# Performance work log

Measured on AMD Instinct MI355X. Metric: run time of the kernel, lower is better.

## Reference

```python
import jax, jax.numpy as jnp
import numpy as np
import math

B, N, DIM, NH, K, PD = 2, 2048, 512, 8, 32, 16
HD = DIM // NH
LN_EPS = 1e-6  # flax LayerNorm default


def _poincare_dist(x, y, c):
    # x, y broadcast to [B, N, N, PD]; returns [B, N, N]
    diff_norm_sq = jnp.sum((x - y) ** 2, axis=-1)
    x_norm_sq = jnp.sum(x ** 2, axis=-1)
    y_norm_sq = jnp.sum(y ** 2, axis=-1)
    den = (1.0 - c * x_norm_sq) * (1.0 - c * y_norm_sq)
    arg = 1.0 + 2.0 * c * diff_norm_sq / jnp.clip(den, 1e-8)
    safe_arg = jnp.maximum(arg, 1.0 + 1e-7)
    return jnp.arccosh(safe_arg) / jnp.sqrt(c)


def _layernorm(x, scale, bias):
    m = jnp.mean(x, axis=-1, keepdims=True)
    v = jnp.var(x, axis=-1, keepdims=True)
    return (x - m) / jnp.sqrt(v + LN_EPS) * scale + bias


def setup_inputs() -> dict:
    key = jax.random.key(0)
    ks = jax.random.split(key, 12)

    def dense(k, din, dout):
        W = jax.random.normal(k, (din, dout), jnp.float32) / np.sqrt(din).astype(np.float32)
        b = jnp.zeros((dout,), jnp.float32)
        return W, b

    inp = {}
    inp["x"] = jax.random.normal(ks[0], (B, N, DIM), jnp.float32)
    # points inside the unit Poincare ball (c=1)
    inp["positions"] = (jax.random.uniform(ks[1], (B, N, PD), jnp.float32) - 0.5) * 0.2
    inp["c"] = jnp.float32(1.0)
    inp["Wq"], inp["bq"] = dense(ks[2], DIM, DIM)
    inp["Wk"], inp["bk"] = dense(ks[3], DIM, DIM)
    inp["Wv"], inp["bv"] = dense(ks[4], DIM, DIM)
    inp["Wo"], inp["bo"] = dense(ks[5], DIM, DIM)
    inp["W1"], inp["b1"] = dense(ks[6], DIM, 4 * DIM)
    inp["W2"], inp["b2"] = dense(ks[7], 4 * DIM, DIM)
    inp["ln1_scale"] = jnp.ones((DIM,), jnp.float32)
    inp["ln1_bias"] = jnp.zeros((DIM,), jnp.float32)
    inp["ln2_scale"] = jnp.ones((DIM,), jnp.float32)
    inp["ln2_bias"] = jnp.zeros((DIM,), jnp.float32)
    inp["log_tau"] = jnp.zeros((1,), jnp.float32)
    inp["attn_scale"] = jnp.ones((1,), jnp.float32)
    return inp


def reference(x, positions, c, Wq, bq, Wk, bk, Wv, bv, Wo, bo,
              W1, b1, W2, b2, ln1_scale, ln1_bias, ln2_scale, ln2_bias,
              log_tau, attn_scale):
    x_res = x
    x_norm = _layernorm(x, ln1_scale, ln1_bias)

    def heads(W, b):
        return (x_norm @ W + b).reshape(B, N, NH, HD).transpose(0, 2, 1, 3)  # [B,H,N,HD]

    q = heads(Wq, bq)
    k = heads(Wk, bk)
    v = heads(Wv, bv)

    # pairwise hyperbolic distances [B,N,N]
    dist_matrix = _poincare_dist(positions[:, None, :, :], positions[:, :, None, :], c)
    _, top_k_indices = jax.lax.top_k(-dist_matrix, K)  # [B,N,K]

    # gather neighbor K/V: out[b,h,i,j,d] = kv[b,h, idx[b,i,j], d]
    gather = jax.vmap(lambda kv_b, idx_b: kv_b[:, idx_b, :])
    k_gathered = gather(k, top_k_indices)  # [B,H,N,K,HD]
    v_gathered = gather(v, top_k_indices)  # [B,H,N,K,HD]

    feature_scores = jnp.einsum('bhid,bhikd->bhik', q, k_gathered) / math.sqrt(HD)
    gathered_dists = jnp.take_along_axis(dist_matrix, top_k_indices, axis=-1)  # [B,N,K]
    geometric_scores = -gathered_dists[:, None, :, :] / jnp.clip(jnp.exp(log_tau), 1e-8)
    attn_scores = attn_scale * jnp.tanh(feature_scores + geometric_scores)
    attn_weights = jax.nn.softmax(attn_scores, axis=-1)

    attn_output = jnp.einsum('bhik,bhikd->bhid', attn_weights, v_gathered)
    attn_output = attn_output.transpose(0, 2, 1, 3).reshape(B, N, DIM)

    x1 = x_res + attn_output @ Wo + bo
    x2_norm = _layernorm(x1, ln2_scale, ln2_bias)
    ffn = jax.nn.gelu(x2_norm @ W1 + b1) @ W2 + b2  # gelu approximate=True (flax default)
    return x1 + ffn
```

## Files before the change

kernel.cpp:

```cpp
#include <hip/hip_runtime.h>
#include <math.h>

#define B_   2
#define N_   2048
#define DIM_ 512
#define NH_  8
#define HD_  64
#define K_   32
#define PD_  16
#define TOK_ (B_*N_)
#define FFN_ 2048
#define QKV_ (3*DIM_)
#define KV_  1024

typedef __bf16 bf16x8 __attribute__((ext_vector_type(8)));
typedef float  f32x4  __attribute__((ext_vector_type(4)));

__device__ __forceinline__ unsigned short f2bf(float f) {
    unsigned int u = __float_as_uint(f);
    u = (u + 0x7fffu + ((u >> 16) & 1u)) >> 16;
    return (unsigned short)u;
}

__device__ __forceinline__ float bflo(unsigned u) { return __uint_as_float(u << 16); }
__device__ __forceinline__ float bfhi(unsigned u) { return __uint_as_float(u & 0xffff0000u); }

__device__ __forceinline__ float gelu_tanh(float x) {
    float x3 = x * x * x;
    return 0.5f * x * (1.f + tanhf(0.7978845608028654f * (x + 0.044715f * x3)));
}

__device__ __forceinline__ float tanh_fast(float x) {
    float e = __expf(2.f * x);
    return 1.f - 2.f / (e + 1.f);
}

__device__ __forceinline__ int lane_mbcnt(unsigned long long m) {
    return __builtin_amdgcn_mbcnt_hi((unsigned)(m >> 32),
           __builtin_amdgcn_mbcnt_lo((unsigned)m, 0));
}

#define GLOAD_LDS16(g, l) __builtin_amdgcn_global_load_lds(                        \
    (const __attribute__((address_space(1))) unsigned int*)(const void*)(g),       \
    (__attribute__((address_space(3))) unsigned int*)(void*)(l), 16, 0, 0)

template<int EPI, int BM, int BN>
__global__ __launch_bounds__(256)
void gemm_bf16_kernel(const unsigned short* __restrict__ A,
                      const unsigned short* __restrict__ Bt,
                      const float* __restrict__ bias,
                      const float* __restrict__ res,
                      float* __restrict__ Cf,
                      unsigned short* __restrict__ Cb,
                      int N, int Kd)
{
    constexpr int WM = BM / 2;
    constexpr int WN = BN / 2;
    constexpr int FM = WM / 16;
    constexpr int FN = WN / 16;
    constexpr int BUFSZ = (BM + BN) * 64;

    __shared__ __align__(16) unsigned short smem[2 * BUFSZ];

    int t    = threadIdx.x;
    int lane = t & 63;
    int wid  = t >> 6;
    int wm   = wid >> 1, wn = wid & 1;
    int bm0  = blockIdx.y * BM;
    int bn0  = blockIdx.x * BN;
    int quad = lane >> 4;
    int rlo  = lane & 15;

    f32x4 acc[FM][FN] = {};

    auto stage = [&](int buf, int k0) {
        unsigned short* As_ = smem + buf * BUFSZ;
        unsigned short* Bs_ = As_ + BM * 64;
#pragma unroll
        for (int l = 0; l < BM/32; l++) {
            int idx = l*256 + t;
            int r   = idx >> 3;
            int g   = (idx & 7) ^ (r & 7);
            GLOAD_LDS16(A + (size_t)(bm0 + r) * Kd + k0 + g*8, As_ + idx*8);
        }
#pragma unroll
        for (int l = 0; l < BN/32; l++) {
            int idx = l*256 + t;
            int r   = idx >> 3;
            int g   = (idx & 7) ^ (r & 7);
            GLOAD_LDS16(Bt + (size_t)(bn0 + r) * Kd + k0 + g*8, Bs_ + idx*8);
        }
    };

    auto compute = [&](int buf) {
        unsigned short* As_ = smem + buf * BUFSZ;
        unsigned short* Bs_ = As_ + BM * 64;
        bf16x8 af[FM][2], bfr[FN][2];
#pragma unroll
        for (int mi = 0; mi < FM; mi++) {
            int r = wm*WM + mi*16 + rlo;
#pragma unroll
            for (int s = 0; s < 2; s++)
                af[mi][s] = *(const bf16x8*)(As_ + r*64 + ((s*4 + quad) ^ (r & 7))*8);
        }
#pragma unroll
        for (int ni = 0; ni < FN; ni++) {
            int r = wn*WN + ni*16 + rlo;
#pragma unroll
            for (int s = 0; s < 2; s++)
                bfr[ni][s] = *(const bf16x8*)(Bs_ + r*64 + ((s*4 + quad) ^ (r & 7))*8);
        }
#pragma unroll
        for (int s = 0; s < 2; s++)
#pragma unroll
            for (int mi = 0; mi < FM; mi++)
#pragma unroll
                for (int ni = 0; ni < FN; ni++)
                    acc[mi][ni] = __builtin_amdgcn_mfma_f32_16x16x32_bf16(
                        af[mi][s], bfr[ni][s], acc[mi][ni], 0, 0, 0);
    };

    stage(0, 0);
    int buf = 0;
    for (int k0 = 0; k0 < Kd; k0 += 64) {
        __syncthreads();
        if (k0 + 64 < Kd) stage(buf ^ 1, k0 + 64);
        compute(buf);
        buf ^= 1;
    }

#pragma unroll
    for (int mi = 0; mi < FM; mi++) {
#pragma unroll
        for (int ni = 0; ni < FN; ni++) {
            int col = bn0 + wn*WN + ni*16 + rlo;
            float bv = bias[col];
#pragma unroll
            for (int r = 0; r < 4; r++) {
                int row = bm0 + wm*WM + mi*16 + quad*4 + r;
                float val = acc[mi][ni][r] + bv;
                if (EPI == 1) val += res[(size_t)row * N + col];
                if (EPI == 2) {
                    val = gelu_tanh(val);
                    Cb[(size_t)row * N + col] = f2bf(val);
                } else if (EPI == 3) {
                    if (col < DIM_) Cf[(size_t)row * DIM_ + col] = val;
                    else            Cb[(size_t)row * KV_ + (col - DIM_)] = f2bf(val);
                } else {
                    Cf[(size_t)row * N + col] = val;
                }
            }
        }
    }
}

__device__ __forceinline__ void extract_row(const unsigned* rb, unsigned T,
                                            int cnt_lt, int m,
                                            unsigned long long* crow,
                                            int hw, int jbase, int lane)
{
    int ltpos = 0;
#pragma unroll
    for (int tt = 0; tt < 16; tt++) {
        bool is_lt = rb[tt] < T;
        unsigned long long mlt = __ballot(is_lt);
        int p = ltpos + lane_mbcnt(mlt);
        if (is_lt) {
            int j = jbase + (tt >> 2)*256 + lane*4 + (tt & 3);
            crow[hw*K_ + p] = ((unsigned long long)rb[tt] << 32) | (unsigned)j;
        }
        ltpos += __popcll(mlt);
    }
    int eqpos = 0;
#pragma unroll
    for (int jg = 0; jg < 4; jg++) {
        bool iseq[4]; unsigned long long meq[4]; int bel[4];
#pragma unroll
        for (int jj = 0; jj < 4; jj++) {
            iseq[jj] = (rb[jg*4+jj] == T);
            meq[jj]  = __ballot(iseq[jj]);
            bel[jj]  = lane_mbcnt(meq[jj]);
        }
        int lane_prefix = bel[0] + bel[1] + bel[2] + bel[3];
        int within = 0;
#pragma unroll
        for (int jj = 0; jj < 4; jj++) {
            int p = eqpos + lane_prefix + within;
            if (iseq[jj] && p < m) {
                int j = jbase + jg*256 + lane*4 + jj;
                crow[hw*K_ + cnt_lt + p] =
                    ((unsigned long long)rb[jg*4+jj] << 32) | (unsigned)j;
            }
            within += iseq[jj] ? 1 : 0;
        }
        eqpos += __popcll(meq[0]) + __popcll(meq[1]) + __popcll(meq[2]) + __popcll(meq[3]);
    }
}

__global__ __launch_bounds__(256)
void dist_topk_kernel(const float* __restrict__ pos,
                      const float* __restrict__ posT,
                      const float* __restrict__ pos_sq,
                      const float* __restrict__ c_ptr,
                      int* __restrict__ topk_idx, float* __restrict__ topk_dist)
{
    __shared__ unsigned long long cand[4][64];

    int wid  = threadIdx.x >> 6;
    int lane = threadIdx.x & 63;
    int rg   = wid >> 1;
    int hw   = wid & 1;
    int bi0  = blockIdx.x * 4 + rg * 2;
    int b    = bi0 >> 11;
    float c  = *c_ptr;
    float inv_sqrt_c = rsqrtf(c);

    float pi0[16], pi1[16];
    {
        const float4* q0 = (const float4*)(pos + (size_t)bi0 * PD_);
        const float4* q1 = (const float4*)(pos + (size_t)(bi0+1) * PD_);
#pragma unroll
        for (int u = 0; u < 4; u++) {
            float4 a = q0[u];
            pi0[4*u]=a.x; pi0[4*u+1]=a.y; pi0[4*u+2]=a.z; pi0[4*u+3]=a.w;
            float4 e = q1[u];
            pi1[4*u]=e.x; pi1[4*u+1]=e.y; pi1[4*u+2]=e.z; pi1[4*u+3]=e.w;
        }
    }
    float om0 = 1.f - c * pos_sq[bi0];
    float om1 = 1.f - c * pos_sq[bi0+1];

    const float* pT  = posT + (size_t)b * 16 * N_;
    const float* sqb = pos_sq + b * N_;
    int jbase = hw * 1024;
    int j0l   = jbase + lane * 4;

    unsigned rb0[16], rb1[16];
#pragma unroll
    for (int jg = 0; jg < 4; jg++) {
        int j0 = j0l + jg * 256;
        float ax=0,ay=0,az=0,aw=0, bx=0,by=0,bz=0,bw=0;
#pragma unroll
        for (int d = 0; d < 16; d++) {
            float4 v = *(const float4*)(pT + d * N_ + j0);
            float d0x = pi0[d]-v.x, d0y = pi0[d]-v.y, d0z = pi0[d]-v.z, d0w = pi0[d]-v.w;
            ax += d0x*d0x; ay += d0y*d0y; az += d0z*d0z; aw += d0w*d0w;
            float d1x = pi1[d]-v.x, d1y = pi1[d]-v.y, d1z = pi1[d]-v.z, d1w = pi1[d]-v.w;
            bx += d1x*d1x; by += d1y*d1y; bz += d1z*d1z; bw += d1w*d1w;
        }
        float4 sq = *(const float4*)(sqb + j0);
        float da[4]={ax,ay,az,aw}, db[4]={bx,by,bz,bw}, sqa[4]={sq.x,sq.y,sq.z,sq.w};
#pragma unroll
        for (int jj = 0; jj < 4; jj++) {
            float omj  = 1.f - c * sqa[jj];
            float den0 = fmaxf(om0 * omj, 1e-8f);
            float den1 = fmaxf(om1 * omj, 1e-8f);
            rb0[jg*4+jj] = __float_as_uint(fmaxf(1.f + 2.f*c*da[jj]/den0, 1.f+1e-7f));
            rb1[jg*4+jj] = __float_as_uint(fmaxf(1.f + 2.f*c*db[jj]/den1, 1.f+1e-7f));
        }
    }

    unsigned T0, T1;
    {
        unsigned band0 = rb0[0], bor0 = rb0[0], band1 = rb1[0], bor1 = rb1[0];
#pragma unroll
        for (int tt = 1; tt < 16; tt++) {
            band0 &= rb0[tt]; bor0 |= rb0[tt];
            band1 &= rb1[tt]; bor1 |= rb1[tt];
        }
#pragma unroll
        for (int off = 32; off; off >>= 1) {
            band0 &= __shfl_xor(band0, off); bor0 |= __shfl_xor(bor0, off);
            band1 &= __shfl_xor(band1, off); bor1 |= __shfl_xor(bor1, off);
        }
        unsigned df0 = band0 ^ bor0, df1 = band1 ^ bor1;
        int hib0 = df0 ? (31 - __clz(df0)) : -1;
        int hib1 = df1 ? (31 - __clz(df1)) : -1;
        int hib  = hib0 > hib1 ? hib0 : hib1;
        T0 = (hib >= 0) ? (band0 & ~((1u << (hib+1)) - 1u)) : band0;
        T1 = (hib >= 0) ? (band1 & ~((1u << (hib+1)) - 1u)) : band1;
        for (int bit = hib; bit >= 0; --bit) {
            unsigned p0 = T0 | (1u << bit), p1 = T1 | (1u << bit);
            int c0 = 0, c1 = 0;
#pragma unroll
            for (int tt = 0; tt < 16; tt++) {
                c0 += __popcll(__ballot(rb0[tt] < p0));
                c1 += __popcll(__ballot(rb1[tt] < p1));
            }
            if (c0 < K_) T0 = p0;
            if (c1 < K_) T1 = p1;
        }
    }
    int cl0 = 0, cl1 = 0;
#pragma unroll
    for (int tt = 0; tt < 16; tt++) {
        cl0 += __popcll(__ballot(rb0[tt] < T0));
        cl1 += __popcll(__ballot(rb1[tt] < T1));
    }

    extract_row(rb0, T0, cl0, K_ - cl0, cand[rg*2+0], hw, jbase, lane);
    extract_row(rb1, T1, cl1, K_ - cl1, cand[rg*2+1], hw, jbase, lane);
    __syncthreads();

    {
        unsigned long long mykey = cand[wid][lane];
        int rank = 0;
#pragma unroll 8
        for (int M = 0; M < 64; M++)
            rank += (cand[wid][M] < mykey) ? 1 : 0;
        if (rank < K_) {
            int bi = blockIdx.x * 4 + wid;
            topk_idx [(size_t)bi * K_ + rank] = (int)(mykey & 0xffffffffu);
            topk_dist[(size_t)bi * K_ + rank] =
                acoshf(__uint_as_float((unsigned)(mykey >> 32))) * inv_sqrt_c;
        }
    }
}

__global__ void fused_prep_kernel(const float* __restrict__ Wq, const float* __restrict__ Wk,
                            const float* __restrict__ Wv, const float* __restrict__ Wo,
                            const float* __restrict__ W1, const float* __restrict__ W2,
                            const float* __restrict__ bq, const float* __restrict__ bk,
                            const float* __restrict__ bv,
                            unsigned short* __restrict__ qkvWt,
                            unsigned short* __restrict__ WoT,
                            unsigned short* __restrict__ W1T,
                            unsigned short* __restrict__ W2T,
                            float* __restrict__ qkv_b,
                            const float* __restrict__ pos,
                            float* __restrict__ pos_sq,
                            float* __restrict__ posT,
                            const float* __restrict__ x,
                            const float* __restrict__ ln1_scale,
                            const float* __restrict__ ln1_bias,
                            unsigned short* __restrict__ xn)
{
    int id = blockIdx.x;
    int t  = threadIdx.x;

    if (id >= 3094) {
        int wave = (id - 3094) * 4 + (t >> 6);
        int lane = t & 63;
        const float* xr = x + (size_t)wave * DIM_;
        float v[8];
        float s = 0.f;
#pragma unroll
        for (int i = 0; i < 8; i++) { v[i] = xr[lane + i*64]; s += v[i]; }
#pragma unroll
        for (int off = 32; off; off >>= 1) s += __shfl_xor(s, off);
        float mean = s * (1.f / DIM_);
        float vs = 0.f;
#pragma unroll
        for (int i = 0; i < 8; i++) { float d = v[i] - mean; vs += d*d; }
#pragma unroll
        for (int off = 32; off; off >>= 1) vs += __shfl_xor(vs, off);
        float inv = rsqrtf(vs * (1.f / DIM_) + 1e-6f);
        unsigned short* yr = xn + (size_t)wave * DIM_;
#pragma unroll
        for (int i = 0; i < 8; i++) {
            int cc = lane + i*64;
            yr[cc] = f2bf((v[i] - mean) * inv * ln1_scale[cc] + ln1_bias[cc]);
        }
        return;
    }
    if (id >= 3078) {
        int i = (id - 3078) * 256 + t;
        int b = i >> 11, j = i & (N_ - 1);
        const float4* p = (const float4*)(pos + (size_t)i * PD_);
        float4 a0 = p[0], a1 = p[1], a2 = p[2], a3 = p[3];
        float pv[16] = {a0.x,a0.y,a0.z,a0.w, a1.x,a1.y,a1.z,a1.w,
                        a2.x,a2.y,a2.z,a2.w, a3.x,a3.y,a3.z,a3.w};
        float s = 0.f;
#pragma unroll
        for (int d = 0; d < 16; d++) s += pv[d]*pv[d];
        pos_sq[i] = s;
        float* pT = posT + (size_t)b * 16 * N_;
#pragma unroll
        for (int d = 0; d < 16; d++) pT[d * N_ + j] = pv[d];
        return;
    }
    if (id >= 3072) {
        int i = (id - 3072) * 256 + t;
        if (i < DIM_)            qkv_b[i] = bq[i];
        else if (i < 2*DIM_)     qkv_b[i] = bk[i - DIM_];
        else                     qkv_b[i] = bv[i - 2*DIM_];
        return;
    }

    const float* W; unsigned short* Wt; int Kd, Nw, nx, ti;
    if      (id < 256)  { W = Wq; Wt = qkvWt;               Kd = 512;  Nw = 512;  nx = 16; ti = id; }
    else if (id < 512)  { W = Wk; Wt = qkvWt + 512*512;     Kd = 512;  Nw = 512;  nx = 16; ti = id - 256; }
    else if (id < 768)  { W = Wv; Wt = qkvWt + 2*512*512;   Kd = 512;  Nw = 512;  nx = 16; ti = id - 512; }
    else if (id < 1024) { W = Wo; Wt = WoT;                 Kd = 512;  Nw = 512;  nx = 16; ti = id - 768; }
    else if (id < 2048) { W = W1; Wt = W1T;                 Kd = 512;  Nw = 2048; nx = 64; ti = id - 1024; }
    else                { W = W2; Wt = W2T;                 Kd = 2048; Nw = 512;  nx = 16; ti = id - 2048; }

    __shared__ float tile[32][33];
    int n0 = (ti % nx) * 32, k0 = (ti / nx) * 32;
    int tx = t & 31, ty = t >> 5;
#pragma unroll
    for (int i = 0; i < 32; i += 8)
        tile[ty + i][tx] = W[(size_t)(k0 + ty + i) * Nw + n0 + tx];
    __syncthreads();
#pragma unroll
    for (int i = 0; i < 32; i += 8)
        Wt[(size_t)(n0 + ty + i) * Kd + k0 + tx] = f2bf(tile[tx][ty + i]);
}

__global__ void layernorm_kernel(const float* __restrict__ x,
                                 const float* __restrict__ scale,
                                 const float* __restrict__ bias,
                                 unsigned short* __restrict__ y)
{
    int wave = (blockIdx.x * blockDim.x + threadIdx.x) >> 6;
    int lane = threadIdx.x & 63;
    if (wave >= TOK_) return;
    const float* xr = x + (size_t)wave * DIM_;
    float v[8];
    float s = 0.f;
#pragma unroll
    for (int i = 0; i < 8; i++) { v[i] = xr[lane + i*64]; s += v[i]; }
#pragma unroll
    for (int off = 32; off; off >>= 1) s += __shfl_xor(s, off);
    float mean = s * (1.f / DIM_);
    float vs = 0.f;
#pragma unroll
    for (int i = 0; i < 8; i++) { float d = v[i] - mean; vs += d*d; }
#pragma unroll
    for (int off = 32; off; off >>= 1) vs += __shfl_xor(vs, off);
    float inv = rsqrtf(vs * (1.f / DIM_) + 1e-6f);
    unsigned short* yr = y + (size_t)wave * DIM_;
#pragma unroll
    for (int i = 0; i < 8; i++) {
        int c = lane + i*64;
        yr[c] = f2bf((v[i] - mean) * inv * scale[c] + bias[c]);
    }
}

__global__ __launch_bounds__(256)
void attn_kernel(const float* __restrict__ q,
                 const unsigned short* __restrict__ kv,
                 const int* __restrict__ topk_idx, const float* __restrict__ topk_dist,
                 const float* __restrict__ log_tau_p, const float* __restrict__ attn_scale_p,
                 unsigned int* __restrict__ out)
{
    int gw   = (blockIdx.x * blockDim.x + threadIdx.x) >> 6;
    int lane = threadIdx.x & 63;
    if (gw >= B_ * NH_ * N_) return;
    int b = gw / (NH_ * N_);
    int r = gw % (NH_ * N_);
    int h = r / N_;
    int i = r % N_;
    int tok = b * N_ + i;

    float tau    = fmaxf(__expf(*log_tau_p), 1e-8f);
    float ascale = *attn_scale_p;

    const int*   idxp = topk_idx  + (size_t)tok * K_;
    const float* dstp = topk_dist + (size_t)tok * K_;
    int   my_idx  = idxp[lane & 31];
    float my_dist = dstp[lane & 31];

    int jj   = lane >> 1;
    int half = lane & 1;

    const float4* qp = (const float4*)(q + (size_t)tok * DIM_ + h * HD_ + half * 32);
    float4 qv[8];
#pragma unroll
    for (int u = 0; u < 8; u++) qv[u] = qp[u];

    int nb = __shfl(my_idx, jj);
    const uint4* kp = (const uint4*)(kv + (size_t)(b * N_ + nb) * KV_ + h * HD_ + half * 32);
    float dot = 0.f;
#pragma unroll
    for (int u = 0; u < 4; u++) {
        uint4 kw = kp[u];
        dot += qv[2*u].x   * bflo(kw.x) + qv[2*u].y   * bfhi(kw.x)
             + qv[2*u].z   * bflo(kw.y) + qv[2*u].w   * bfhi(kw.y)
             + qv[2*u+1].x * bflo(kw.z) + qv[2*u+1].y * bfhi(kw.z)
             + qv[2*u+1].z * bflo(kw.w) + qv[2*u+1].w * bfhi(kw.w);
    }
    dot += __shfl_xor(dot, 1);

    float fs = dot * 0.125f;
    float gs = -__shfl(my_dist, jj) / tau;
    float s  = ascale * tanh_fast(fs + gs);

    float mx = s;
#pragma unroll
    for (int off = 32; off; off >>= 1) mx = fmaxf(mx, __shfl_xor(mx, off));
    float e  = __expf(s - mx);
    float ec = half ? 0.f : e;
#pragma unroll
    for (int off = 32; off; off >>= 1) ec += __shfl_xor(ec, off);
    float inv = 1.f / ec;

    int dp    = lane & 31;
    int half2 = lane >> 5;
    const unsigned int* vb = (const unsigned int*)(kv + DIM_ + h * HD_) + dp;
    float ax = 0.f, ay = 0.f;
#pragma unroll
    for (int it = 0; it < 16; it++) {
        int t2 = half2 + 2*it;
        float w  = __shfl(e, t2 * 2) * inv;
        int   nj = __shfl(my_idx, t2);
        unsigned vv = vb[(size_t)(b * N_ + nj) * (KV_/2)];
        ax += w * bflo(vv);
        ay += w * bfhi(vv);
    }
    ax += __shfl_xor(ax, 32);
    ay += __shfl_xor(ay, 32);
    if (lane < 32) {
        unsigned pck = ((unsigned)f2bf(ay) << 16) | (unsigned)f2bf(ax);
        out[(size_t)tok * (DIM_/2) + h * (HD_/2) + dp] = pck;
    }
}

extern "C" void kernel_launch(void* const* d_in, const int* in_sizes, int n_in,
                              void* d_out, int out_size, void* d_ws, size_t ws_size,
                              hipStream_t stream)
{
    const float* x          = (const float*)d_in[0];
    const float* positions  = (const float*)d_in[1];
    const float* c_p        = (const float*)d_in[2];
    const float* Wq         = (const float*)d_in[3];
    const float* bq         = (const float*)d_in[4];
    const float* Wk         = (const float*)d_in[5];
    const float* bk         = (const float*)d_in[6];
    const float* Wv         = (const float*)d_in[7];
    const float* bv         = (const float*)d_in[8];
    const float* Wo         = (const float*)d_in[9];
    const float* bo         = (const float*)d_in[10];
    const float* W1         = (const float*)d_in[11];
    const float* b1         = (const float*)d_in[12];
    const float* W2         = (const float*)d_in[13];
    const float* b2         = (const float*)d_in[14];
    const float* ln1_scale  = (const float*)d_in[15];
    const float* ln1_bias   = (const float*)d_in[16];
    const float* ln2_scale  = (const float*)d_in[17];
    const float* ln2_bias   = (const float*)d_in[18];
    const float* log_tau    = (const float*)d_in[19];
    const float* attn_scale = (const float*)d_in[20];

    char* p = (char*)d_ws;
    unsigned short* qkvWt  = (unsigned short*)p; p += (size_t)QKV_ * DIM_ * 2;
    unsigned short* WoT    = (unsigned short*)p; p += (size_t)DIM_ * DIM_ * 2;
    unsigned short* W1T    = (unsigned short*)p; p += (size_t)FFN_ * DIM_ * 2;
    unsigned short* W2T    = (unsigned short*)p; p += (size_t)DIM_ * FFN_ * 2;
    float*          qkv_b  = (float*)p;          p += (size_t)QKV_ * 4;
    unsigned short* xn     = (unsigned short*)p; p += (size_t)TOK_ * DIM_ * 2;
    float*          qf     = (float*)p;          p += (size_t)TOK_ * DIM_ * 4;
    unsigned short* kvb    = (unsigned short*)p; p += (size_t)TOK_ * KV_ * 2;
    unsigned short* attn_o = (unsigned short*)p; p += (size_t)TOK_ * DIM_ * 2;
    float*          x1     = (float*)p;          p += (size_t)TOK_ * DIM_ * 4;
    unsigned short* x2n    = (unsigned short*)p; p += (size_t)TOK_ * DIM_ * 2;
    unsigned short* hbuf   = (unsigned short*)p; p += (size_t)TOK_ * FFN_ * 2;
    float*          pos_sq = (float*)p;          p += (size_t)TOK_ * 4;
    float*          posT   = (float*)p;          p += (size_t)B_ * 16 * N_ * 4;
    float*          tk_d   = (float*)p;          p += (size_t)TOK_ * K_ * 4;
    int*            tk_i   = (int*)p;            p += (size_t)TOK_ * K_ * 4;

    fused_prep_kernel<<<4118, 256, 0, stream>>>(Wq, Wk, Wv, Wo, W1, W2, bq, bk, bv,
                                                qkvWt, WoT, W1T, W2T, qkv_b,
                                                positions, pos_sq, posT,
                                                x, ln1_scale, ln1_bias, xn);

    gemm_bf16_kernel<3,64,128><<<dim3(QKV_/128, TOK_/64), 256, 0, stream>>>(
        xn, qkvWt, qkv_b, nullptr, qf, kvb, QKV_, DIM_);

    dist_topk_kernel<<<TOK_/4, 256, 0, stream>>>(positions, posT, pos_sq,
                                                 c_p, tk_i, tk_d);

    attn_kernel<<<(B_*NH_*N_)/4, 256, 0, stream>>>(qf, kvb, tk_i, tk_d,
                                                   log_tau, attn_scale,
                                                   (unsigned int*)attn_o);

    gemm_bf16_kernel<1,64,64><<<dim3(DIM_/64, TOK_/64), 256, 0, stream>>>(
        attn_o, WoT, bo, x, x1, nullptr, DIM_, DIM_);

    layernorm_kernel<<<TOK_/4, 256, 0, stream>>>(x1, ln2_scale, ln2_bias, x2n);

    gemm_bf16_kernel<2,64,128><<<dim3(FFN_/128, TOK_/64), 256, 0, stream>>>(
        x2n, W1T, b1, nullptr, nullptr, hbuf, FFN_, DIM_);

    gemm_bf16_kernel<1,64,64><<<dim3(DIM_/64, TOK_/64), 256, 0, stream>>>(
        hbuf, W2T, b2, x1, (float*)d_out, nullptr, DIM_, FFN_);
}
```

Before: 244.4 us.

## Process four query rows per wave in distance top-k kernel

Each wave in the distance/top-k kernel now handles four query rows instead of two, so one block covers eight rows and the grid is halved. Every posT column load is reused across four rows, and the per-row position values are made wave-uniform with readfirstlane so they can sit in scalar registers. This cuts global loads per row and the number of blocks. In exchange the radix-select ballots are interleaved across four rows, register pressure rises sharply (four 16-entry key arrays per lane), and occupancy may drop.

```diff
diff --git a/kernel.cpp b/kernel.cpp
--- a/kernel.cpp
+++ b/kernel.cpp
@@ -24,6 +24,11 @@
 
 __device__ __forceinline__ float bflo(unsigned u) { return __uint_as_float(u << 16); }
 __device__ __forceinline__ float bfhi(unsigned u) { return __uint_as_float(u & 0xffff0000u); }
+
+__device__ __forceinline__ float rfl_f32(float x) {
+    return __uint_as_float(
+        (unsigned)__builtin_amdgcn_readfirstlane((int)__float_as_uint(x)));
+}
 
 __device__ __forceinline__ float gelu_tanh(float x) {
     float x3 = x * x * x;
@@ -204,112 +209,128 @@
                       const float* __restrict__ c_ptr,
                       int* __restrict__ topk_idx, float* __restrict__ topk_dist)
 {
-    __shared__ unsigned long long cand[4][64];
+    __shared__ unsigned long long cand[8][64];
 
     int wid  = threadIdx.x >> 6;
     int lane = threadIdx.x & 63;
     int rg   = wid >> 1;
     int hw   = wid & 1;
-    int bi0  = blockIdx.x * 4 + rg * 2;
-    int b    = bi0 >> 11;
+    int base = blockIdx.x * 8 + rg * 4;
+    int b    = base >> 11;
     float c  = *c_ptr;
     float inv_sqrt_c = rsqrtf(c);
 
-    float pi0[16], pi1[16];
-    {
-        const float4* q0 = (const float4*)(pos + (size_t)bi0 * PD_);
-        const float4* q1 = (const float4*)(pos + (size_t)(bi0+1) * PD_);
+    float pv[4][16];
+    float om[4];
+#pragma unroll
+    for (int r = 0; r < 4; r++) {
+        const float4* pp = (const float4*)(pos + (size_t)(base + r) * PD_);
 #pragma unroll
         for (int u = 0; u < 4; u++) {
-            float4 a = q0[u];
-            pi0[4*u]=a.x; pi0[4*u+1]=a.y; pi0[4*u+2]=a.z; pi0[4*u+3]=a.w;
-            float4 e = q1[u];
-            pi1[4*u]=e.x; pi1[4*u+1]=e.y; pi1[4*u+2]=e.z; pi1[4*u+3]=e.w;
-        }
-    }
-    float om0 = 1.f - c * pos_sq[bi0];
-    float om1 = 1.f - c * pos_sq[bi0+1];
+            float4 a = pp[u];
+            pv[r][4*u+0] = rfl_f32(a.x);
+            pv[r][4*u+1] = rfl_f32(a.y);
+            pv[r][4*u+2] = rfl_f32(a.z);
+            pv[r][4*u+3] = rfl_f32(a.w);
+        }
+        om[r] = 1.f - c * rfl_f32(pos_sq[base + r]);
+    }
 
     const float* pT  = posT + (size_t)b * 16 * N_;
     const float* sqb = pos_sq + b * N_;
     int jbase = hw * 1024;
     int j0l   = jbase + lane * 4;
 
-    unsigned rb0[16], rb1[16];
+    unsigned rb[4][16];
 #pragma unroll
     for (int jg = 0; jg < 4; jg++) {
         int j0 = j0l + jg * 256;
-        float ax=0,ay=0,az=0,aw=0, bx=0,by=0,bz=0,bw=0;
+        f32x4 df[4] = {};
 #pragma unroll
         for (int d = 0; d < 16; d++) {
             float4 v = *(const float4*)(pT + d * N_ + j0);
-            float d0x = pi0[d]-v.x, d0y = pi0[d]-v.y, d0z = pi0[d]-v.z, d0w = pi0[d]-v.w;
-            ax += d0x*d0x; ay += d0y*d0y; az += d0z*d0z; aw += d0w*d0w;
-            float d1x = pi1[d]-v.x, d1y = pi1[d]-v.y, d1z = pi1[d]-v.z, d1w = pi1[d]-v.w;
-            bx += d1x*d1x; by += d1y*d1y; bz += d1z*d1z; bw += d1w*d1w;
+#pragma unroll
+            for (int r = 0; r < 4; r++) {
+                float dx = pv[r][d]-v.x, dy = pv[r][d]-v.y,
+                      dz = pv[r][d]-v.z, dw = pv[r][d]-v.w;
+                df[r][0] += dx*dx; df[r][1] += dy*dy;
+                df[r][2] += dz*dz; df[r][3] += dw*dw;
+            }
         }
         float4 sq = *(const float4*)(sqb + j0);
-        float da[4]={ax,ay,az,aw}, db[4]={bx,by,bz,bw}, sqa[4]={sq.x,sq.y,sq.z,sq.w};
+        float sqa[4] = {sq.x, sq.y, sq.z, sq.w};
 #pragma unroll
         for (int jj = 0; jj < 4; jj++) {
-            float omj  = 1.f - c * sqa[jj];
-            float den0 = fmaxf(om0 * omj, 1e-8f);
-            float den1 = fmaxf(om1 * omj, 1e-8f);
-            rb0[jg*4+jj] = __float_as_uint(fmaxf(1.f + 2.f*c*da[jj]/den0, 1.f+1e-7f));
-            rb1[jg*4+jj] = __float_as_uint(fmaxf(1.f + 2.f*c*db[jj]/den1, 1.f+1e-7f));
-        }
-    }
-
-    unsigned T0, T1;
+            float omj = 1.f - c * sqa[jj];
+#pragma unroll
+            for (int r = 0; r < 4; r++) {
+                float den = fmaxf(om[r] * omj, 1e-8f);
+                rb[r][jg*4+jj] =
+                    __float_as_uint(fmaxf(1.f + 2.f*c*df[r][jj]/den, 1.f+1e-7f));
+            }
+        }
+    }
+
+    unsigned T[4];
     {
-        unsigned band0 = rb0[0], bor0 = rb0[0], band1 = rb1[0], bor1 = rb1[0];
-#pragma unroll
-        for (int tt = 1; tt < 16; tt++) {
-            band0 &= rb0[tt]; bor0 |= rb0[tt];
-            band1 &= rb1[tt]; bor1 |= rb1[tt];
-        }
-#pragma unroll
-        for (int off = 32; off; off >>= 1) {
-            band0 &= __shfl_xor(band0, off); bor0 |= __shfl_xor(bor0, off);
-            band1 &= __shfl_xor(band1, off); bor1 |= __shfl_xor(bor1, off);
-        }
-        unsigned df0 = band0 ^ bor0, df1 = band1 ^ bor1;
-        int hib0 = df0 ? (31 - __clz(df0)) : -1;
-        int hib1 = df1 ? (31 - __clz(df1)) : -1;
-        int hib  = hib0 > hib1 ? hib0 : hib1;
-        T0 = (hib >= 0) ? (band0 & ~((1u << (hib+1)) - 1u)) : band0;
-        T1 = (hib >= 0) ? (band1 & ~((1u << (hib+1)) - 1u)) : band1;
+        unsigned band[4], bor[4];
+#pragma unroll
+        for (int r = 0; r < 4; r++) { band[r] = rb[r][0]; bor[r] = rb[r][0]; }
+#pragma unroll
+        for (int tt = 1; tt < 16; tt++)
+#pragma unroll
+            for (int r = 0; r < 4; r++) { band[r] &= rb[r][tt]; bor[r] |= rb[r][tt]; }
+#pragma unroll
+        for (int off = 32; off; off >>= 1)
+#pragma unroll
+            for (int r = 0; r < 4; r++) {
+                band[r] &= __shfl_xor(band[r], off);
+                bor[r]  |= __shfl_xor(bor[r],  off);
+            }
+        int hib = -1;
+#pragma unroll
+        for (int r = 0; r < 4; r++) {
+            unsigned df = band[r] ^ bor[r];
+            int h = df ? (31 - __clz(df)) : -1;
+            hib = h > hib ? h : hib;
+        }
+#pragma unroll
+        for (int r = 0; r < 4; r++)
+            T[r] = (hib >= 0) ? (band[r] & ~((1u << (hib+1)) - 1u)) : band[r];
         for (int bit = hib; bit >= 0; --bit) {
-            unsigned p0 = T0 | (1u << bit), p1 = T1 | (1u << bit);
-            int c0 = 0, c1 = 0;
-#pragma unroll
-            for (int tt = 0; tt < 16; tt++) {
-                c0 += __popcll(__ballot(rb0[tt] < p0));
-                c1 += __popcll(__ballot(rb1[tt] < p1));
-            }
-            if (c0 < K_) T0 = p0;
-            if (c1 < K_) T1 = p1;
-        }
-    }
-    int cl0 = 0, cl1 = 0;
-#pragma unroll
-    for (int tt = 0; tt < 16; tt++) {
-        cl0 += __popcll(__ballot(rb0[tt] < T0));
-        cl1 += __popcll(__ballot(rb1[tt] < T1));
-    }
-
-    extract_row(rb0, T0, cl0, K_ - cl0, cand[rg*2+0], hw, jbase, lane);
-    extract_row(rb1, T1, cl1, K_ - cl1, cand[rg*2+1], hw, jbase, lane);
+            int cnt[4] = {};
+#pragma unroll
+            for (int tt = 0; tt < 16; tt++)
+#pragma unroll
+                for (int r = 0; r < 4; r++)
+                    cnt[r] += __popcll(__ballot(rb[r][tt] < (T[r] | (1u << bit))));
+#pragma unroll
+            for (int r = 0; r < 4; r++)
+                if (cnt[r] < K_) T[r] |= (1u << bit);
+        }
+    }
+    int cl[4] = {};
+#pragma unroll
+    for (int tt = 0; tt < 16; tt++)
+#pragma unroll
+        for (int r = 0; r < 4; r++)
+            cl[r] += __popcll(__ballot(rb[r][tt] < T[r]));
+
+#pragma unroll
+    for (int r = 0; r < 4; r++)
+        extract_row(rb[r], T[r], cl[r], K_ - cl[r], cand[rg*4 + r], hw, jbase, lane);
     __syncthreads();
 
-    {
-        unsigned long long mykey = cand[wid][lane];
+#pragma unroll
+    for (int rr = 0; rr < 2; rr++) {
+        int row = wid * 2 + rr;
+        unsigned long long mykey = cand[row][lane];
         int rank = 0;
 #pragma unroll 8
         for (int M = 0; M < 64; M++)
-            rank += (cand[wid][M] < mykey) ? 1 : 0;
+            rank += (cand[row][M] < mykey) ? 1 : 0;
         if (rank < K_) {
-            int bi = blockIdx.x * 4 + wid;
+            int bi = blockIdx.x * 8 + row;
             topk_idx [(size_t)bi * K_ + rank] = (int)(mykey & 0xffffffffu);
             topk_dist[(size_t)bi * K_ + rank] =
                 acoshf(__uint_as_float((unsigned)(mykey >> 32))) * inv_sqrt_c;
@@ -568,7 +589,7 @@
     gemm_bf16_kernel<3,64,128><<<dim3(QKV_/128, TOK_/64), 256, 0, stream>>>(
         xn, qkvWt, qkv_b, nullptr, qf, kvb, QKV_, DIM_);
 
-    dist_topk_kernel<<<TOK_/4, 256, 0, stream>>>(positions, posT, pos_sq,
+    dist_topk_kernel<<<TOK_/8, 256, 0, stream>>>(positions, posT, pos_sq,
                                                  c_p, tk_i, tk_d);
 
     attn_kernel<<<(B_*NH_*N_)/4, 256, 0, stream>>>(qf, kvb, tk_i, tk_d,
```

After: 258.6 us. +5.8%, slower.
